# Optimization experiments

Measured on AMD Instinct MI355X. Metric: run time of the kernel, lower is better.

Reference implementation:

```python
import jax, jax.numpy as jnp
import numpy as np

RES = 512
MAX_DEPTH = 100.0
AMBIENT = 0.3
LIGHT_STREN = 0.8
SHININESS = 16.0
EPS = 1e-8


def _unit(v):
    return v / (jnp.linalg.norm(v, axis=-1, keepdims=True) + EPS)


def setup_inputs() -> dict:
    key = jax.random.key(0)
    ks = jax.random.split(key, 8)
    B, N, M, TEX = 1, 512, 128, 512
    verts = jax.random.uniform(ks[0], (B, N, 3), minval=-1.0, maxval=1.0, dtype=jnp.float32)
    faces = jax.random.randint(ks[1], (B, M, 3), 0, N, dtype=jnp.int32)
    normals = jax.random.normal(ks[2], (B, M, 3, 3), dtype=jnp.float32)
    uvs = jax.random.uniform(ks[3], (B, M, 3, 2), dtype=jnp.float32)
    textures = jax.random.uniform(ks[4], (B, TEX, TEX, 3), dtype=jnp.float32)
    f = RES / 2.0
    K = jnp.array([[f, 0.0, RES / 2.0], [0.0, f, RES / 2.0], [0.0, 0.0, 1.0]], jnp.float32)
    Ks = jnp.broadcast_to(K, (B, 3, 3))
    RT = jnp.concatenate([jnp.eye(3, dtype=jnp.float32), jnp.array([[0.0], [0.0], [2.0]], jnp.float32)], axis=1)
    RTs = jnp.broadcast_to(RT, (B, 3, 4))
    view_dir = jax.random.normal(ks[5], (B, 3), dtype=jnp.float32)
    light_dir = jax.random.normal(ks[6], (B, 3), dtype=jnp.float32)
    return {"verts": verts, "faces": faces, "normals": normals, "uvs": uvs,
            "textures": textures, "Ks": Ks, "RTs": RTs, "view_dir": view_dir, "light_dir": light_dir}


def _render(verts, faces, normals, uvs, textures, Ks, RTs, view_dir, light_dir):
    B = verts.shape[0]
    # camera space: cam = R @ v + t
    cam = jnp.einsum('bij,bnj->bni', RTs[:, :, :3], verts) + RTs[:, None, :, 3]
    # orthographic projection to pixel coords
    x = Ks[:, None, 0, 0] * cam[..., 0] + Ks[:, None, 0, 2]
    y = Ks[:, None, 1, 1] * cam[..., 1] + Ks[:, None, 1, 2]
    xy = jnp.stack([x, y], -1)            # [B,N,2]
    z = cam[..., 2]                        # [B,N]
    gather_v = jax.vmap(lambda a, f: a[f])
    tv = gather_v(xy, faces)               # [B,M,3,2] screen-space triangle corners
    tz = gather_v(z, faces)                # [B,M,3]
    # pixel centers, row-major (p = row*RES + col)
    ii = jnp.arange(RES, dtype=jnp.float32) + 0.5
    py, px = jnp.meshgrid(ii, ii, indexing='ij')
    pix = jnp.stack([px.ravel(), py.ravel()], -1)   # [P,2]

    def edge(a, b, p):
        return (b[..., 0] - a[..., 0]) * (p[..., 1] - a[..., 1]) - (b[..., 1] - a[..., 1]) * (p[..., 0] - a[..., 0])

    v0, v1, v2 = tv[:, None, :, 0], tv[:, None, :, 1], tv[:, None, :, 2]  # [B,1,M,2]
    p = pix[None, :, None]                                               # [1,P,1,2]
    w0 = edge(v1, v2, p)                   # [B,P,M]
    w1 = edge(v2, v0, p)
    w2 = edge(v0, v1, p)
    area = w0 + w1 + w2
    inside = (((w0 >= 0) & (w1 >= 0) & (w2 >= 0)) | ((w0 <= 0) & (w1 <= 0) & (w2 <= 0))) & (jnp.abs(area) > EPS)
    inv_a = 1.0 / jnp.where(jnp.abs(area) > EPS, area, 1.0)
    zpix = (w0 * tz[:, None, :, 0] + w1 * tz[:, None, :, 1] + w2 * tz[:, None, :, 2]) * inv_a
    valid = inside & (zpix > 0)
    zc = jnp.where(valid, zpix, MAX_DEPTH)   # [B,P,M] candidate depths
    depth = jnp.min(zc, axis=-1)             # z-buffer result [B,P]
    win = jnp.argmin(zc, axis=-1)             # winning triangle per pixel [B,P]
    hit = depth < MAX_DEPTH

    # recompute barycentrics for the winning triangle only (avoids [B,P,M,3])
    gpick = jax.vmap(lambda a, i: a[i])
    tvw = gpick(tv, win)                      # [B,P,3,2]
    nw = gpick(normals, win)                  # [B,P,3,3]
    uvw = gpick(uvs, win)                     # [B,P,3,2]
    pp = pix[None]                            # [1,P,2]

    def e2(a, b):
        return (b[..., 0] - a[..., 0]) * (pp[..., 1] - a[..., 1]) - (b[..., 1] - a[..., 1]) * (pp[..., 0] - a[..., 0])

    u0 = e2(tvw[:, :, 1], tvw[:, :, 2])
    u1 = e2(tvw[:, :, 2], tvw[:, :, 0])
    u2 = e2(tvw[:, :, 0], tvw[:, :, 1])
    ar = u0 + u1 + u2
    inv2 = 1.0 / jnp.where(jnp.abs(ar) > EPS, ar, 1.0)
    bary = jnp.stack([u0, u1, u2], -1) * inv2[..., None]   # [B,P,3]
    nrm = _unit(jnp.einsum('bpk,bpkc->bpc', bary, nw))     # interpolated normal
    uv = jnp.einsum('bpk,bpkc->bpc', bary, uvw)            # interpolated uv [B,P,2]

    # bilinear texture sampling
    Ht, Wt = textures.shape[1], textures.shape[2]
    uu = jnp.clip(uv[..., 0], 0.0, 1.0) * (Wt - 1)
    vv = jnp.clip(uv[..., 1], 0.0, 1.0) * (Ht - 1)
    x0 = jnp.floor(uu).astype(jnp.int32)
    y0 = jnp.floor(vv).astype(jnp.int32)
    x1 = jnp.minimum(x0 + 1, Wt - 1)
    y1 = jnp.minimum(y0 + 1, Ht - 1)
    fx = (uu - x0.astype(jnp.float32))[..., None]
    fy = (vv - y0.astype(jnp.float32))[..., None]
    tget = jax.vmap(lambda t, a, b: t[a, b])
    col = (tget(textures, y0, x0) * (1 - fx) * (1 - fy) + tget(textures, y0, x1) * fx * (1 - fy)
           + tget(textures, y1, x0) * (1 - fx) * fy + tget(textures, y1, x1) * fx * fy)  # [B,P,3]

    # Lambert diffuse + Blinn-Phong specular
    ld = _unit(light_dir)
    vd = _unit(view_dir)
    diff = jnp.clip(jnp.einsum('bpc,bc->bp', nrm, ld), 0.0)
    h = _unit(ld + vd)
    spec = LIGHT_STREN * jnp.clip(jnp.einsum('bpc,bc->bp', nrm, h), 0.0) ** SHININESS
    shade = col * (AMBIENT + LIGHT_STREN * diff)[..., None] + spec[..., None]
    rgb = jnp.where(hit[..., None], shade, 0.0)

    depths = depth.reshape(B, RES, RES)
    rgbs = rgb.reshape(B, RES, RES, 3)
    masks = hit.reshape(B, RES, RES).astype(jnp.int32)
    return depths, rgbs, masks


def reference(verts, faces, normals, uvs, textures, Ks, RTs, view_dir, light_dir):
    return _render(verts, faces, normals, uvs, textures, Ks, RTs, view_dir, light_dir)
```

## Files before the change

kernel.cpp:

```cpp
#include <hip/hip_runtime.h>
#include <math.h>

#pragma clang fp contract(off)

#define RES         512
#define TILE        16
#define TILESX      (RES / TILE)
#define MAXF        128
#define MAX_DEPTH   100.0f
#define AMBIENT     0.3f
#define LIGHT_STREN 0.8f
#define EPSF        1e-8f
#define MARG        1.0f
#define ZGUARD      1e-3f

struct __attribute__((packed, aligned(4))) PF4 { float a, b, c, d; };
struct __attribute__((packed, aligned(4))) PF2 { float a, b; };
static __device__ __forceinline__ PF4 ld4(const float* p) { PF4 v; __builtin_memcpy(&v, p, 16); return v; }
static __device__ __forceinline__ PF2 ld2(const float* p) { PF2 v; __builtin_memcpy(&v, p, 8); return v; }

__global__ __launch_bounds__(256) void mesh_render_tiled(
    const float* __restrict__ verts,
    const int*   __restrict__ faces,
    const float* __restrict__ normals,
    const float* __restrict__ uvs,
    const float* __restrict__ tex,
    const float* __restrict__ Ks,
    const float* __restrict__ RTs,
    const float* __restrict__ view_dir,
    const float* __restrict__ light_dir,
    float* __restrict__ out,
    int M, int TEXW, int TEXH)
{
    __shared__ float4 smA[MAXF];
    __shared__ float4 smB[MAXF];
    __shared__ float2 smC[MAXF];
    __shared__ int    cid[MAXF];
    __shared__ int    scnt[2][8];
    __shared__ float  slit[6];

    const int tid = threadIdx.x;
    const int tx  = blockIdx.x % TILESX;
    const int ty  = blockIdx.x / TILESX;
    const float PX0 = (float)(tx * TILE) + 0.5f;
    const float PY0 = (float)(ty * TILE) + 0.5f;

    bool flag = false;
    int  bkt  = -1;
    float X0=0,Y0=0,Z0=0, X1=0,Y1=0,Z1=0, X2=0,Y2=0,Z2=0, MZ=0;
    unsigned long long bmask = 0;

    if (tid < MAXF) {
        if (tid < M) {
            const float r00 = RTs[0], r01 = RTs[1], r02 = RTs[2],  t0 = RTs[3];
            const float r10 = RTs[4], r11 = RTs[5], r12 = RTs[6],  t1 = RTs[7];
            const float r20 = RTs[8], r21 = RTs[9], r22 = RTs[10], t2 = RTs[11];
            const float k00 = Ks[0], k02 = Ks[2], k11 = Ks[4], k12 = Ks[5];
            float X[3], Y[3], Z[3];
            #pragma unroll
            for (int k = 0; k < 3; ++k) {
                int vi = faces[tid * 3 + k];
                float vx = verts[vi * 3 + 0];
                float vy = verts[vi * 3 + 1];
                float vz = verts[vi * 3 + 2];
                float cx = ((r00 * vx + r01 * vy) + r02 * vz) + t0;
                float cy = ((r10 * vx + r11 * vy) + r12 * vz) + t1;
                float cz = ((r20 * vx + r21 * vy) + r22 * vz) + t2;
                X[k] = k00 * cx + k02;
                Y[k] = k11 * cy + k12;
                Z[k] = cz;
            }
            X0=X[0]; Y0=Y[0]; Z0=Z[0]; X1=X[1]; Y1=Y[1]; Z1=Z[1];
            X2=X[2]; Y2=Y[2]; Z2=Z[2];
            MZ = fminf(fminf(Z0, Z1), Z2);

            float e0dx = X2-X1, e0dy = Y2-Y1;
            float e1dx = X0-X2, e1dy = Y0-Y2;
            float e2dx = X1-X0, e2dy = Y1-Y0;

            float minX = fminf(fminf(X0,X1),X2), maxX = fmaxf(fmaxf(X0,X1),X2);
            float minY = fminf(fminf(Y0,Y1),Y2), maxY = fmaxf(fmaxf(Y0,Y1),Y2);
            bool bb = (minX <= PX0 + 15.0f + MARG) && (maxX >= PX0 - MARG) &&
                      (minY <= PY0 + 15.0f + MARG) && (maxY >= PY0 - MARG);

            float wA0 = e0dx*(PY0-Y1) - e0dy*(PX0-X1);
            float wA1 = e1dx*(PY0-Y2) - e1dy*(PX0-X2);
            float wA2 = e2dx*(PY0-Y0) - e2dy*(PX0-X0);
            float area = (wA0 + wA1) + wA2;
            float amin = fminf(area, 0.0f) - MARG, amax = fmaxf(area, 0.0f) + MARG;

            float s0x = -e0dy*15.0f, s0y = e0dx*15.0f;
            float s1x = -e1dy*15.0f, s1y = e1dx*15.0f;
            float s2x = -e2dy*15.0f, s2y = e2dx*15.0f;
            float t0min = wA0 + fminf(s0x,0.f) + fminf(s0y,0.f);
            float t0max = wA0 + fmaxf(s0x,0.f) + fmaxf(s0y,0.f);
            float t1min = wA1 + fminf(s1x,0.f) + fminf(s1y,0.f);
            float t1max = wA1 + fmaxf(s1x,0.f) + fmaxf(s1y,0.f);
            float t2min = wA2 + fminf(s2x,0.f) + fminf(s2y,0.f);
            float t2max = wA2 + fmaxf(s2x,0.f) + fmaxf(s2y,0.f);
            bool ok0 = (t0max >= amin) && (t0min <= amax);
            bool ok1 = (t1max >= amin) && (t1min <= amax);
            bool ok2 = (t2max >= amin) && (t2min <= amax);
            flag = bb && ok0 && ok1 && ok2;
            if (flag) {
                int bq = (int)((MZ - 1.0f) * 4.0f);
                bkt = bq < 0 ? 0 : (bq > 7 ? 7 : bq);
            }
        }
        #pragma unroll
        for (int k = 0; k < 8; ++k) {
            unsigned long long mk = __ballot(flag && (bkt == k));
            if (bkt == k) bmask = mk;
            if ((tid & 63) == 0) scnt[tid >> 6][k] = __popcll(mk);
        }
    }
    if (tid == 128) {
        float lx = light_dir[0], ly = light_dir[1], lz = light_dir[2];
        float ll = sqrtf((lx*lx + ly*ly) + lz*lz) + 1e-8f;
        lx /= ll; ly /= ll; lz /= ll;
        float vx = view_dir[0], vy = view_dir[1], vz = view_dir[2];
        float vl = sqrtf((vx*vx + vy*vy) + vz*vz) + 1e-8f;
        vx /= vl; vy /= vl; vz /= vl;
        float hx = lx + vx, hy = ly + vy, hz = lz + vz;
        float hl = sqrtf((hx*hx + hy*hy) + hz*hz) + 1e-8f;
        slit[0] = lx; slit[1] = ly; slit[2] = lz;
        slit[3] = hx / hl; slit[4] = hy / hl; slit[5] = hz / hl;
    }
    __syncthreads();

    if (flag) {
        int wv = tid >> 6;
        int base = 0;
        for (int k = 0; k < bkt; ++k) base += scnt[0][k] + scnt[1][k];
        if (wv == 1) base += scnt[0][bkt];
        int pos = base + __popcll(bmask & ((1ull << (tid & 63)) - 1ull));
        smA[pos] = make_float4(X0, Y0, X1, Y1);
        smB[pos] = make_float4(X2, Y2, Z0, Z1);
        smC[pos] = make_float2(MZ - ZGUARD, Z2);
        cid[pos] = tid;
    }
    __syncthreads();

    int bend[8];
    {
        int acc = 0;
        #pragma unroll
        for (int k = 0; k < 8; ++k) { acc += scnt[0][k] + scnt[1][k]; bend[k] = acc; }
    }

    const int lx_ = tid & (TILE-1), ly_ = tid / TILE;
    const float px = PX0 + (float)lx_;
    const float py = PY0 + (float)ly_;
    const int p = (ty*TILE + ly_) * RES + (tx*TILE + lx_);

    float best = MAX_DEPTH;
    float w0s = 0.0f, w1s = 0.0f, w2s = 0.0f, invs = 1.0f;
    int winpos = -1;

    int i = 0;
    #pragma unroll 1
    for (int k = 0; k < 8; ++k) {
        const int e = bend[k];
        if (i >= e) continue;
        float lbk = (1.0f + 0.25f * (float)k) - ZGUARD;
        if (__all(lbk >= best)) break;
        for (; i < e; ++i) {
            const float2 c = smC[i];
            if (__all(c.x >= best)) continue;
            const float4 A = smA[i];
            const float4 B = smB[i];
            float w0 = (B.x - A.z) * (py - A.w) - (B.y - A.w) * (px - A.z);
            float w1 = (A.x - B.x) * (py - B.y) - (A.y - B.y) * (px - B.x);
            float w2 = (A.z - A.x) * (py - A.y) - (A.w - A.y) * (px - A.x);
            float area = (w0 + w1) + w2;
            float mn = fminf(fminf(w0, w1), w2);
            float mx = fmaxf(fmaxf(w0, w1), w2);
            bool nz = fabsf(area) > EPSF;
            bool inside = ((mn >= 0.0f) || (mx <= 0.0f)) && nz;
            float inva = __builtin_amdgcn_rcpf(nz ? area : 1.0f);
            float zpix = ((w0 * B.z + w1 * B.w) + w2 * c.y) * inva;
            float zc = (inside && (zpix > 0.0f)) ? zpix : MAX_DEPTH;
            if (zc < best) {
                best = zc; winpos = i;
                w0s = w0; w1s = w1; w2s = w2; invs = inva;
            }
        }
    }

    float r = 0.0f, g = 0.0f, b = 0.0f, mk = 0.0f, depth = MAX_DEPTH;
    if (winpos >= 0) {
        mk = 1.0f;
        depth = best;
        const int f = cid[winpos];
        float b0 = w0s * invs, b1 = w1s * invs, b2 = w2s * invs;

        const float* nw = normals + f * 9;
        PF4 n0 = ld4(nw); PF4 n1 = ld4(nw + 4); float n8 = nw[8];
        float nx  = (b0 * n0.a + b1 * n0.d) + b2 * n1.c;
        float ny  = (b0 * n0.b + b1 * n1.a) + b2 * n1.d;
        float nzv = (b0 * n0.c + b1 * n1.b) + b2 * n8;
        float nl  = __builtin_amdgcn_sqrtf((nx*nx + ny*ny) + nzv*nzv) + 1e-8f;
        float rn  = __builtin_amdgcn_rcpf(nl);
        nx *= rn; ny *= rn; nzv *= rn;

        const float* uvp = uvs + f * 6;
        PF4 u0 = ld4(uvp); PF2 u1 = ld2(uvp + 4);
        float uvx = (b0 * u0.a + b1 * u0.c) + b2 * u1.a;
        float uvy = (b0 * u0.b + b1 * u0.d) + b2 * u1.b;
        float uu = fminf(fmaxf(uvx, 0.0f), 1.0f) * (float)(TEXW - 1);
        float vv = fminf(fmaxf(uvy, 0.0f), 1.0f) * (float)(TEXH - 1);
        int x0 = (int)floorf(uu), y0 = (int)floorf(vv);
        int y1 = min(y0 + 1, TEXH - 1);
        float fx = uu - (float)x0, fy = vv - (float)y0;

        int xb = min(x0, TEXW - 2);
        bool xe = (x0 == TEXW - 1);
        const float* r0 = tex + (y0 * TEXW + xb) * 3;
        const float* r1 = tex + (y1 * TEXW + xb) * 3;
        PF4 a0 = ld4(r0); PF2 a1 = ld2(r0 + 4);
        PF4 c0 = ld4(r1); PF2 c1 = ld2(r1 + 4);
        float t00r = xe ? a0.d : a0.a, t00g = xe ? a1.a : a0.b, t00b = xe ? a1.b : a0.c;
        float t01r = a0.d,             t01g = a1.a,             t01b = a1.b;
        float t10r = xe ? c0.d : c0.a, t10g = xe ? c1.a : c0.b, t10b = xe ? c1.b : c0.c;
        float t11r = c0.d,             t11g = c1.a,             t11b = c1.b;

        float gx = 1.0f - fx, gy = 1.0f - fy;
        float cr = (((t00r*gx)*gy + (t01r*fx)*gy) + (t10r*gx)*fy) + (t11r*fx)*fy;
        float cg = (((t00g*gx)*gy + (t01g*fx)*gy) + (t10g*gx)*fy) + (t11g*fx)*fy;
        float cb = (((t00b*gx)*gy + (t01b*fx)*gy) + (t10b*gx)*fy) + (t11b*fx)*fy;

        float ldx = slit[0], ldy = slit[1], ldz = slit[2];
        float hx  = slit[3], hy  = slit[4], hz  = slit[5];
        float diff = fmaxf((nx*ldx + ny*ldy) + nzv*ldz, 0.0f);
        float sd   = fmaxf((nx*hx  + ny*hy)  + nzv*hz,  0.0f);
        float s2 = sd*sd, s4 = s2*s2, s8 = s4*s4, s16 = s8*s8;
        float spec  = LIGHT_STREN * s16;
        float scale = AMBIENT + LIGHT_STREN * diff;
        r = cr * scale + spec;
        g = cg * scale + spec;
        b = cb * scale + spec;
    }

    out[p] = depth;
    struct F3 { float x, y, z; };
    ((F3*)(out + RES * RES))[p] = F3{r, g, b};
    out[RES * RES * 4 + p] = mk;
}

extern "C" void kernel_launch(void* const* d_in, const int* in_sizes, int n_in,
                              void* d_out, int out_size, void* d_ws, size_t ws_size,
                              hipStream_t stream) {
    const float* verts     = (const float*)d_in[0];
    const int*   faces     = (const int*)  d_in[1];
    const float* normals   = (const float*)d_in[2];
    const float* uvs       = (const float*)d_in[3];
    const float* tex       = (const float*)d_in[4];
    const float* Ks        = (const float*)d_in[5];
    const float* RTs       = (const float*)d_in[6];
    const float* view_dir  = (const float*)d_in[7];
    const float* light_dir = (const float*)d_in[8];

    int M = in_sizes[1] / 3;
    if (M > MAXF) M = MAXF;
    const int texels = in_sizes[4] / 3;
    const int TEXW = (int)(sqrt((double)texels) + 0.5);
    const int TEXH = TEXW;

    const int blocks = TILESX * TILESX;
    mesh_render_tiled<<<blocks, 256, 0, stream>>>(
        verts, faces, normals, uvs, tex, Ks, RTs, view_dir, light_dir,
        (float*)d_out, M, TEXW, TEXH);
}
```

Before: 16.21 us.

## Split vertex transform into prepass kernel and rasterize 8x8 tiles with single-wave blocks

```diff
diff --git a/kernel.cpp b/kernel.cpp
--- a/kernel.cpp
+++ b/kernel.cpp
@@ -4,7 +4,7 @@
 #pragma clang fp contract(off)
 
 #define RES         512
-#define TILE        16
+#define TILE        8
 #define TILESX      (RES / TILE)
 #define MAXF        128
 #define MAX_DEPTH   100.0f
@@ -13,20 +13,51 @@
 #define EPSF        1e-8f
 #define MARG        1.0f
 #define ZGUARD      1e-3f
+#define EXT         7.0f
 
 struct __attribute__((packed, aligned(4))) PF4 { float a, b, c, d; };
 struct __attribute__((packed, aligned(4))) PF2 { float a, b; };
 static __device__ __forceinline__ PF4 ld4(const float* p) { PF4 v; __builtin_memcpy(&v, p, 16); return v; }
 static __device__ __forceinline__ PF2 ld2(const float* p) { PF2 v; __builtin_memcpy(&v, p, 8); return v; }
 
-__global__ __launch_bounds__(256) void mesh_render_tiled(
-    const float* __restrict__ verts,
-    const int*   __restrict__ faces,
+__global__ __launch_bounds__(128) void xform_faces(
+    const float* __restrict__ verts, const int* __restrict__ faces,
+    const float* __restrict__ Ks, const float* __restrict__ RTs,
+    float4* __restrict__ ws, int M)
+{
+    const int f = threadIdx.x;
+    if (f >= M) return;
+    const float r00 = RTs[0], r01 = RTs[1], r02 = RTs[2],  t0 = RTs[3];
+    const float r10 = RTs[4], r11 = RTs[5], r12 = RTs[6],  t1 = RTs[7];
+    const float r20 = RTs[8], r21 = RTs[9], r22 = RTs[10], t2 = RTs[11];
+    const float k00 = Ks[0], k02 = Ks[2], k11 = Ks[4], k12 = Ks[5];
+    float X[3], Y[3], Z[3];
+    #pragma unroll
+    for (int k = 0; k < 3; ++k) {
+        int vi = faces[f * 3 + k];
+        float vx = verts[vi * 3 + 0];
+        float vy = verts[vi * 3 + 1];
+        float vz = verts[vi * 3 + 2];
+        float cx = ((r00 * vx + r01 * vy) + r02 * vz) + t0;
+        float cy = ((r10 * vx + r11 * vy) + r12 * vz) + t1;
+        float cz = ((r20 * vx + r21 * vy) + r22 * vz) + t2;
+        X[k] = k00 * cx + k02;
+        Y[k] = k11 * cy + k12;
+        Z[k] = cz;
+    }
+    float MZ = fminf(fminf(Z[0], Z[1]), Z[2]);
+    int bq = (int)((MZ - 1.0f) * 4.0f);
+    int bkt = bq < 0 ? 0 : (bq > 7 ? 7 : bq);
+    ws[f * 3 + 0] = make_float4(X[0], Y[0], X[1], Y[1]);
+    ws[f * 3 + 1] = make_float4(X[2], Y[2], Z[0], Z[1]);
+    ws[f * 3 + 2] = make_float4(MZ - ZGUARD, Z[2], (float)bkt, 0.0f);
+}
+
+__global__ __launch_bounds__(64) void raster_tiles(
+    const float4* __restrict__ ws,
     const float* __restrict__ normals,
     const float* __restrict__ uvs,
     const float* __restrict__ tex,
-    const float* __restrict__ Ks,
-    const float* __restrict__ RTs,
     const float* __restrict__ view_dir,
     const float* __restrict__ light_dir,
     float* __restrict__ out,
@@ -36,117 +67,76 @@
     __shared__ float4 smB[MAXF];
     __shared__ float2 smC[MAXF];
     __shared__ int    cid[MAXF];
-    __shared__ int    scnt[2][8];
-    __shared__ float  slit[6];
 
     const int tid = threadIdx.x;
-    const int tx  = blockIdx.x % TILESX;
+    const int tx  = blockIdx.x & (TILESX - 1);
     const int ty  = blockIdx.x / TILESX;
     const float PX0 = (float)(tx * TILE) + 0.5f;
     const float PY0 = (float)(ty * TILE) + 0.5f;
 
-    bool flag = false;
-    int  bkt  = -1;
-    float X0=0,Y0=0,Z0=0, X1=0,Y1=0,Z1=0, X2=0,Y2=0,Z2=0, MZ=0;
-    unsigned long long bmask = 0;
-
-    if (tid < MAXF) {
-        if (tid < M) {
-            const float r00 = RTs[0], r01 = RTs[1], r02 = RTs[2],  t0 = RTs[3];
-            const float r10 = RTs[4], r11 = RTs[5], r12 = RTs[6],  t1 = RTs[7];
-            const float r20 = RTs[8], r21 = RTs[9], r22 = RTs[10], t2 = RTs[11];
-            const float k00 = Ks[0], k02 = Ks[2], k11 = Ks[4], k12 = Ks[5];
-            float X[3], Y[3], Z[3];
-            #pragma unroll
-            for (int k = 0; k < 3; ++k) {
-                int vi = faces[tid * 3 + k];
-                float vx = verts[vi * 3 + 0];
-                float vy = verts[vi * 3 + 1];
-                float vz = verts[vi * 3 + 2];
-                float cx = ((r00 * vx + r01 * vy) + r02 * vz) + t0;
-                float cy = ((r10 * vx + r11 * vy) + r12 * vz) + t1;
-                float cz = ((r20 * vx + r21 * vy) + r22 * vz) + t2;
-                X[k] = k00 * cx + k02;
-                Y[k] = k11 * cy + k12;
-                Z[k] = cz;
-            }
-            X0=X[0]; Y0=Y[0]; Z0=Z[0]; X1=X[1]; Y1=Y[1]; Z1=Z[1];
-            X2=X[2]; Y2=Y[2]; Z2=Z[2];
-            MZ = fminf(fminf(Z0, Z1), Z2);
-
-            float e0dx = X2-X1, e0dy = Y2-Y1;
-            float e1dx = X0-X2, e1dy = Y0-Y2;
-            float e2dx = X1-X0, e2dy = Y1-Y0;
-
-            float minX = fminf(fminf(X0,X1),X2), maxX = fmaxf(fmaxf(X0,X1),X2);
-            float minY = fminf(fminf(Y0,Y1),Y2), maxY = fmaxf(fmaxf(Y0,Y1),Y2);
-            bool bb = (minX <= PX0 + 15.0f + MARG) && (maxX >= PX0 - MARG) &&
-                      (minY <= PY0 + 15.0f + MARG) && (maxY >= PY0 - MARG);
-
-            float wA0 = e0dx*(PY0-Y1) - e0dy*(PX0-X1);
-            float wA1 = e1dx*(PY0-Y2) - e1dy*(PX0-X2);
-            float wA2 = e2dx*(PY0-Y0) - e2dy*(PX0-X0);
-            float area = (wA0 + wA1) + wA2;
-            float amin = fminf(area, 0.0f) - MARG, amax = fmaxf(area, 0.0f) + MARG;
-
-            float s0x = -e0dy*15.0f, s0y = e0dx*15.0f;
-            float s1x = -e1dy*15.0f, s1y = e1dx*15.0f;
-            float s2x = -e2dy*15.0f, s2y = e2dx*15.0f;
-            float t0min = wA0 + fminf(s0x,0.f) + fminf(s0y,0.f);
-            float t0max = wA0 + fmaxf(s0x,0.f) + fmaxf(s0y,0.f);
-            float t1min = wA1 + fminf(s1x,0.f) + fminf(s1y,0.f);
-            float t1max = wA1 + fmaxf(s1x,0.f) + fmaxf(s1y,0.f);
-            float t2min = wA2 + fminf(s2x,0.f) + fminf(s2y,0.f);
-            float t2max = wA2 + fmaxf(s2x,0.f) + fmaxf(s2y,0.f);
-            bool ok0 = (t0max >= amin) && (t0min <= amax);
-            bool ok1 = (t1max >= amin) && (t1min <= amax);
-            bool ok2 = (t2max >= amin) && (t2min <= amax);
-            flag = bb && ok0 && ok1 && ok2;
-            if (flag) {
-                int bq = (int)((MZ - 1.0f) * 4.0f);
-                bkt = bq < 0 ? 0 : (bq > 7 ? 7 : bq);
-            }
-        }
-        #pragma unroll
-        for (int k = 0; k < 8; ++k) {
-            unsigned long long mk = __ballot(flag && (bkt == k));
-            if (bkt == k) bmask = mk;
-            if ((tid & 63) == 0) scnt[tid >> 6][k] = __popcll(mk);
-        }
-    }
-    if (tid == 128) {
-        float lx = light_dir[0], ly = light_dir[1], lz = light_dir[2];
-        float ll = sqrtf((lx*lx + ly*ly) + lz*lz) + 1e-8f;
-        lx /= ll; ly /= ll; lz /= ll;
-        float vx = view_dir[0], vy = view_dir[1], vz = view_dir[2];
-        float vl = sqrtf((vx*vx + vy*vy) + vz*vz) + 1e-8f;
-        vx /= vl; vy /= vl; vz /= vl;
-        float hx = lx + vx, hy = ly + vy, hz = lz + vz;
-        float hl = sqrtf((hx*hx + hy*hy) + hz*hz) + 1e-8f;
-        slit[0] = lx; slit[1] = ly; slit[2] = lz;
-        slit[3] = hx / hl; slit[4] = hy / hl; slit[5] = hz / hl;
-    }
+    const int f0 = tid, f1 = tid + 64;
+    float4 A0 = ws[f0 * 3 + 0], B0 = ws[f0 * 3 + 1], C0 = ws[f0 * 3 + 2];
+    float4 A1, B1, C1;
+    bool have1 = (f1 < M);
+    if (have1) { A1 = ws[f1 * 3 + 0]; B1 = ws[f1 * 3 + 1]; C1 = ws[f1 * 3 + 2]; }
+
+    auto sat = [&](const float4& A, const float4& B) -> bool {
+        float e0dx = B.x - A.z, e0dy = B.y - A.w;
+        float e1dx = A.x - B.x, e1dy = A.y - B.y;
+        float e2dx = A.z - A.x, e2dy = A.w - A.y;
+        float minX = fminf(fminf(A.x, A.z), B.x), maxX = fmaxf(fmaxf(A.x, A.z), B.x);
+        float minY = fminf(fminf(A.y, A.w), B.y), maxY = fmaxf(fmaxf(A.y, A.w), B.y);
+        bool bb = (minX <= PX0 + EXT + MARG) && (maxX >= PX0 - MARG) &&
+                  (minY <= PY0 + EXT + MARG) && (maxY >= PY0 - MARG);
+        float wA0 = e0dx*(PY0 - A.w) - e0dy*(PX0 - A.z);
+        float wA1 = e1dx*(PY0 - B.y) - e1dy*(PX0 - B.x);
+        float wA2 = e2dx*(PY0 - A.y) - e2dy*(PX0 - A.x);
+        float area = (wA0 + wA1) + wA2;
+        float amin = fminf(area, 0.0f) - MARG, amax = fmaxf(area, 0.0f) + MARG;
+        float s0x = -e0dy*EXT, s0y = e0dx*EXT;
+        float s1x = -e1dy*EXT, s1y = e1dx*EXT;
+        float s2x = -e2dy*EXT, s2y = e2dx*EXT;
+        float t0mn = wA0 + fminf(s0x,0.f) + fminf(s0y,0.f);
+        float t0mx = wA0 + fmaxf(s0x,0.f) + fmaxf(s0y,0.f);
+        float t1mn = wA1 + fminf(s1x,0.f) + fminf(s1y,0.f);
+        float t1mx = wA1 + fmaxf(s1x,0.f) + fmaxf(s1y,0.f);
+        float t2mn = wA2 + fminf(s2x,0.f) + fminf(s2y,0.f);
+        float t2mx = wA2 + fmaxf(s2x,0.f) + fmaxf(s2y,0.f);
+        bool ok0 = (t0mx >= amin) && (t0mn <= amax);
+        bool ok1 = (t1mx >= amin) && (t1mn <= amax);
+        bool ok2 = (t2mx >= amin) && (t2mn <= amax);
+        return bb && ok0 && ok1 && ok2;
+    };
+    bool flag0 = (f0 < M) && sat(A0, B0);
+    bool flag1 = have1 && sat(A1, B1);
+    int bkt0 = flag0 ? (int)C0.z : -1;
+    int bkt1 = flag1 ? (int)C1.z : -1;
+
+    const unsigned long long lt = (1ull << tid) - 1ull;
+    int posA = -1, posB = -1, bend[8];
+    int acc = 0;
+    #pragma unroll
+    for (int k = 0; k < 8; ++k) {
+        unsigned long long mA = __ballot(bkt0 == k);
+        unsigned long long mB = __ballot(bkt1 == k);
+        if (bkt0 == k) posA = acc + __popcll(mA & lt);
+        if (bkt1 == k) posB = acc + __popcll(mA) + __popcll(mB & lt);
+        acc += __popcll(mA) + __popcll(mB);
+        bend[k] = acc;
+    }
+    if (posA >= 0) { smA[posA]=A0; smB[posA]=B0; smC[posA]=make_float2(C0.x,C0.y); cid[posA]=f0; }
+    if (posB >= 0) { smA[posB]=A1; smB[posB]=B1; smC[posB]=make_float2(C1.x,C1.y); cid[posB]=f1; }
     __syncthreads();
 
-    if (flag) {
-        int wv = tid >> 6;
-        int base = 0;
-        for (int k = 0; k < bkt; ++k) base += scnt[0][k] + scnt[1][k];
-        if (wv == 1) base += scnt[0][bkt];
-        int pos = base + __popcll(bmask & ((1ull << (tid & 63)) - 1ull));
-        smA[pos] = make_float4(X0, Y0, X1, Y1);
-        smB[pos] = make_float4(X2, Y2, Z0, Z1);
-        smC[pos] = make_float2(MZ - ZGUARD, Z2);
-        cid[pos] = tid;
-    }
-    __syncthreads();
-
-    int bend[8];
-    {
-        int acc = 0;
-        #pragma unroll
-        for (int k = 0; k < 8; ++k) { acc += scnt[0][k] + scnt[1][k]; bend[k] = acc; }
-    }
+    float ldx = light_dir[0], ldy = light_dir[1], ldz = light_dir[2];
+    float ll = sqrtf((ldx*ldx + ldy*ldy) + ldz*ldz) + 1e-8f;
+    ldx /= ll; ldy /= ll; ldz /= ll;
+    float vx = view_dir[0], vy = view_dir[1], vz = view_dir[2];
+    float vl = sqrtf((vx*vx + vy*vy) + vz*vz) + 1e-8f;
+    vx /= vl; vy /= vl; vz /= vl;
+    float hx = ldx + vx, hy = ldy + vy, hz = ldz + vz;
+    float hl = sqrtf((hx*hx + hy*hy) + hz*hz) + 1e-8f;
+    hx /= hl; hy /= hl; hz /= hl;
 
     const int lx_ = tid & (TILE-1), ly_ = tid / TILE;
     const float px = PX0 + (float)lx_;
@@ -229,8 +219,6 @@
         float cg = (((t00g*gx)*gy + (t01g*fx)*gy) + (t10g*gx)*fy) + (t11g*fx)*fy;
         float cb = (((t00b*gx)*gy + (t01b*fx)*gy) + (t10b*gx)*fy) + (t11b*fx)*fy;
 
-        float ldx = slit[0], ldy = slit[1], ldz = slit[2];
-        float hx  = slit[3], hy  = slit[4], hz  = slit[5];
         float diff = fmaxf((nx*ldx + ny*ldy) + nzv*ldz, 0.0f);
         float sd   = fmaxf((nx*hx  + ny*hy)  + nzv*hz,  0.0f);
         float s2 = sd*sd, s4 = s2*s2, s8 = s4*s4, s16 = s8*s8;
@@ -266,8 +254,10 @@
     const int TEXW = (int)(sqrt((double)texels) + 0.5);
     const int TEXH = TEXW;
 
+    float4* ws = (float4*)d_ws;
+    xform_faces<<<1, 128, 0, stream>>>(verts, faces, Ks, RTs, ws, M);
     const int blocks = TILESX * TILESX;
-    mesh_render_tiled<<<blocks, 256, 0, stream>>>(
-        verts, faces, normals, uvs, tex, Ks, RTs, view_dir, light_dir,
+    raster_tiles<<<blocks, 64, 0, stream>>>(
+        ws, normals, uvs, tex, view_dir, light_dir,
         (float*)d_out, M, TEXW, TEXH);
 }
```

Result: slower. 20.84 us (+28.6%).

## Halve block size, shade two pixels per thread, stage verts/faces in LDS

Applied to the files above, without the earlier changes.

```diff
diff --git a/kernel.cpp b/kernel.cpp
--- a/kernel.cpp
+++ b/kernel.cpp
@@ -7,6 +7,7 @@
 #define TILE        16
 #define TILESX      (RES / TILE)
 #define MAXF        128
+#define MAXV        512
 #define MAX_DEPTH   100.0f
 #define AMBIENT     0.3f
 #define LIGHT_STREN 0.8f
@@ -19,7 +20,7 @@
 static __device__ __forceinline__ PF4 ld4(const float* p) { PF4 v; __builtin_memcpy(&v, p, 16); return v; }
 static __device__ __forceinline__ PF2 ld2(const float* p) { PF2 v; __builtin_memcpy(&v, p, 8); return v; }
 
-__global__ __launch_bounds__(256) void mesh_render_tiled(
+__global__ __launch_bounds__(128) void mesh_render_tiled(
     const float* __restrict__ verts,
     const int*   __restrict__ faces,
     const float* __restrict__ normals,
@@ -30,14 +31,15 @@
     const float* __restrict__ view_dir,
     const float* __restrict__ light_dir,
     float* __restrict__ out,
-    int M, int TEXW, int TEXH)
+    int M, int NV, int TEXW, int TEXH)
 {
+    __shared__ float sverts[MAXV * 3];
+    __shared__ int   sfaces[MAXF * 3];
     __shared__ float4 smA[MAXF];
     __shared__ float4 smB[MAXF];
     __shared__ float2 smC[MAXF];
     __shared__ int    cid[MAXF];
     __shared__ int    scnt[2][8];
-    __shared__ float  slit[6];
 
     const int tid = threadIdx.x;
     const int tx  = blockIdx.x % TILESX;
@@ -45,86 +47,90 @@
     const float PX0 = (float)(tx * TILE) + 0.5f;
     const float PY0 = (float)(ty * TILE) + 0.5f;
 
+    {
+        const int nvf = NV * 3;
+        const int nv4 = nvf >> 2;
+        const float4* v4 = (const float4*)verts;
+        for (int idx = tid; idx < nv4; idx += 128)
+            ((float4*)sverts)[idx] = v4[idx];
+        for (int idx = (nv4 << 2) + tid; idx < nvf; idx += 128)
+            sverts[idx] = verts[idx];
+        const int nff = M * 3;
+        const int nf4 = nff >> 2;
+        const int4* f4 = (const int4*)faces;
+        for (int idx = tid; idx < nf4; idx += 128)
+            ((int4*)sfaces)[idx] = f4[idx];
+        for (int idx = (nf4 << 2) + tid; idx < nff; idx += 128)
+            sfaces[idx] = faces[idx];
+    }
+    __syncthreads();
+
     bool flag = false;
     int  bkt  = -1;
     float X0=0,Y0=0,Z0=0, X1=0,Y1=0,Z1=0, X2=0,Y2=0,Z2=0, MZ=0;
     unsigned long long bmask = 0;
 
-    if (tid < MAXF) {
-        if (tid < M) {
-            const float r00 = RTs[0], r01 = RTs[1], r02 = RTs[2],  t0 = RTs[3];
-            const float r10 = RTs[4], r11 = RTs[5], r12 = RTs[6],  t1 = RTs[7];
-            const float r20 = RTs[8], r21 = RTs[9], r22 = RTs[10], t2 = RTs[11];
-            const float k00 = Ks[0], k02 = Ks[2], k11 = Ks[4], k12 = Ks[5];
-            float X[3], Y[3], Z[3];
-            #pragma unroll
-            for (int k = 0; k < 3; ++k) {
-                int vi = faces[tid * 3 + k];
-                float vx = verts[vi * 3 + 0];
-                float vy = verts[vi * 3 + 1];
-                float vz = verts[vi * 3 + 2];
-                float cx = ((r00 * vx + r01 * vy) + r02 * vz) + t0;
-                float cy = ((r10 * vx + r11 * vy) + r12 * vz) + t1;
-                float cz = ((r20 * vx + r21 * vy) + r22 * vz) + t2;
-                X[k] = k00 * cx + k02;
-                Y[k] = k11 * cy + k12;
-                Z[k] = cz;
-            }
-            X0=X[0]; Y0=Y[0]; Z0=Z[0]; X1=X[1]; Y1=Y[1]; Z1=Z[1];
-            X2=X[2]; Y2=Y[2]; Z2=Z[2];
-            MZ = fminf(fminf(Z0, Z1), Z2);
-
-            float e0dx = X2-X1, e0dy = Y2-Y1;
-            float e1dx = X0-X2, e1dy = Y0-Y2;
-            float e2dx = X1-X0, e2dy = Y1-Y0;
-
-            float minX = fminf(fminf(X0,X1),X2), maxX = fmaxf(fmaxf(X0,X1),X2);
-            float minY = fminf(fminf(Y0,Y1),Y2), maxY = fmaxf(fmaxf(Y0,Y1),Y2);
-            bool bb = (minX <= PX0 + 15.0f + MARG) && (maxX >= PX0 - MARG) &&
-                      (minY <= PY0 + 15.0f + MARG) && (maxY >= PY0 - MARG);
-
-            float wA0 = e0dx*(PY0-Y1) - e0dy*(PX0-X1);
-            float wA1 = e1dx*(PY0-Y2) - e1dy*(PX0-X2);
-            float wA2 = e2dx*(PY0-Y0) - e2dy*(PX0-X0);
-            float area = (wA0 + wA1) + wA2;
-            float amin = fminf(area, 0.0f) - MARG, amax = fmaxf(area, 0.0f) + MARG;
-
-            float s0x = -e0dy*15.0f, s0y = e0dx*15.0f;
-            float s1x = -e1dy*15.0f, s1y = e1dx*15.0f;
-            float s2x = -e2dy*15.0f, s2y = e2dx*15.0f;
-            float t0min = wA0 + fminf(s0x,0.f) + fminf(s0y,0.f);
-            float t0max = wA0 + fmaxf(s0x,0.f) + fmaxf(s0y,0.f);
-            float t1min = wA1 + fminf(s1x,0.f) + fminf(s1y,0.f);
-            float t1max = wA1 + fmaxf(s1x,0.f) + fmaxf(s1y,0.f);
-            float t2min = wA2 + fminf(s2x,0.f) + fminf(s2y,0.f);
-            float t2max = wA2 + fmaxf(s2x,0.f) + fmaxf(s2y,0.f);
-            bool ok0 = (t0max >= amin) && (t0min <= amax);
-            bool ok1 = (t1max >= amin) && (t1min <= amax);
-            bool ok2 = (t2max >= amin) && (t2min <= amax);
-            flag = bb && ok0 && ok1 && ok2;
-            if (flag) {
-                int bq = (int)((MZ - 1.0f) * 4.0f);
-                bkt = bq < 0 ? 0 : (bq > 7 ? 7 : bq);
-            }
+    if (tid < M) {
+        const float r00 = RTs[0], r01 = RTs[1], r02 = RTs[2],  t0 = RTs[3];
+        const float r10 = RTs[4], r11 = RTs[5], r12 = RTs[6],  t1 = RTs[7];
+        const float r20 = RTs[8], r21 = RTs[9], r22 = RTs[10], t2 = RTs[11];
+        const float k00 = Ks[0], k02 = Ks[2], k11 = Ks[4], k12 = Ks[5];
+        float X[3], Y[3], Z[3];
+        #pragma unroll
+        for (int k = 0; k < 3; ++k) {
+            int vi = sfaces[tid * 3 + k];
+            float vx = sverts[vi * 3 + 0];
+            float vy = sverts[vi * 3 + 1];
+            float vz = sverts[vi * 3 + 2];
+            float cx = ((r00 * vx + r01 * vy) + r02 * vz) + t0;
+            float cy = ((r10 * vx + r11 * vy) + r12 * vz) + t1;
+            float cz = ((r20 * vx + r21 * vy) + r22 * vz) + t2;
+            X[k] = k00 * cx + k02;
+            Y[k] = k11 * cy + k12;
+            Z[k] = cz;
         }
-        #pragma unroll
-        for (int k = 0; k < 8; ++k) {
-            unsigned long long mk = __ballot(flag && (bkt == k));
-            if (bkt == k) bmask = mk;
-            if ((tid & 63) == 0) scnt[tid >> 6][k] = __popcll(mk);
+        X0=X[0]; Y0=Y[0]; Z0=Z[0]; X1=X[1]; Y1=Y[1]; Z1=Z[1];
+        X2=X[2]; Y2=Y[2]; Z2=Z[2];
+        MZ = fminf(fminf(Z0, Z1), Z2);
+
+        float e0dx = X2-X1, e0dy = Y2-Y1;
+        float e1dx = X0-X2, e1dy = Y0-Y2;
+        float e2dx = X1-X0, e2dy = Y1-Y0;
+
+        float minX = fminf(fminf(X0,X1),X2), maxX = fmaxf(fmaxf(X0,X1),X2);
+        float minY = fminf(fminf(Y0,Y1),Y2), maxY = fmaxf(fmaxf(Y0,Y1),Y2);
+        bool bb = (minX <= PX0 + 15.0f + MARG) && (maxX >= PX0 - MARG) &&
+                  (minY <= PY0 + 15.0f + MARG) && (maxY >= PY0 - MARG);
+
+        float wA0 = e0dx*(PY0-Y1) - e0dy*(PX0-X1);
+        float wA1 = e1dx*(PY0-Y2) - e1dy*(PX0-X2);
+        float wA2 = e2dx*(PY0-Y0) - e2dy*(PX0-X0);
+        float area = (wA0 + wA1) + wA2;
+        float amin = fminf(area, 0.0f) - MARG, amax = fmaxf(area, 0.0f) + MARG;
+
+        float s0x = -e0dy*15.0f, s0y = e0dx*15.0f;
+        float s1x = -e1dy*15.0f, s1y = e1dx*15.0f;
+        float s2x = -e2dy*15.0f, s2y = e2dx*15.0f;
+        float t0mn = wA0 + fminf(s0x,0.f) + fminf(s0y,0.f);
+        float t0mx = wA0 + fmaxf(s0x,0.f) + fmaxf(s0y,0.f);
+        float t1mn = wA1 + fminf(s1x,0.f) + fminf(s1y,0.f);
+        float t1mx = wA1 + fmaxf(s1x,0.f) + fmaxf(s1y,0.f);
+        float t2mn = wA2 + fminf(s2x,0.f) + fminf(s2y,0.f);
+        float t2mx = wA2 + fmaxf(s2x,0.f) + fmaxf(s2y,0.f);
+        bool ok0 = (t0mx >= amin) && (t0mn <= amax);
+        bool ok1 = (t1mx >= amin) && (t1mn <= amax);
+        bool ok2 = (t2mx >= amin) && (t2mn <= amax);
+        flag = bb && ok0 && ok1 && ok2;
+        if (flag) {
+            int bq = (int)((MZ - 1.0f) * 4.0f);
+            bkt = bq < 0 ? 0 : (bq > 7 ? 7 : bq);
         }
     }
-    if (tid == 128) {
-        float lx = light_dir[0], ly = light_dir[1], lz = light_dir[2];
-        float ll = sqrtf((lx*lx + ly*ly) + lz*lz) + 1e-8f;
-        lx /= ll; ly /= ll; lz /= ll;
-        float vx = view_dir[0], vy = view_dir[1], vz = view_dir[2];
-        float vl = sqrtf((vx*vx + vy*vy) + vz*vz) + 1e-8f;
-        vx /= vl; vy /= vl; vz /= vl;
-        float hx = lx + vx, hy = ly + vy, hz = lz + vz;
-        float hl = sqrtf((hx*hx + hy*hy) + hz*hz) + 1e-8f;
-        slit[0] = lx; slit[1] = ly; slit[2] = lz;
-        slit[3] = hx / hl; slit[4] = hy / hl; slit[5] = hz / hl;
+    #pragma unroll
+    for (int k = 0; k < 8; ++k) {
+        unsigned long long mk = __ballot(flag && (bkt == k));
+        if (bkt == k) bmask = mk;
+        if ((tid & 63) == 0) scnt[tid >> 6][k] = __popcll(mk);
     }
     __syncthreads();
 
@@ -148,14 +154,27 @@
         for (int k = 0; k < 8; ++k) { acc += scnt[0][k] + scnt[1][k]; bend[k] = acc; }
     }
 
-    const int lx_ = tid & (TILE-1), ly_ = tid / TILE;
-    const float px = PX0 + (float)lx_;
-    const float py = PY0 + (float)ly_;
-    const int p = (ty*TILE + ly_) * RES + (tx*TILE + lx_);
-
-    float best = MAX_DEPTH;
-    float w0s = 0.0f, w1s = 0.0f, w2s = 0.0f, invs = 1.0f;
-    int winpos = -1;
+    float ldx = light_dir[0], ldy = light_dir[1], ldz = light_dir[2];
+    float ll = sqrtf((ldx*ldx + ldy*ldy) + ldz*ldz) + 1e-8f;
+    ldx /= ll; ldy /= ll; ldz /= ll;
+    float vdx = view_dir[0], vdy = view_dir[1], vdz = view_dir[2];
+    float vl = sqrtf((vdx*vdx + vdy*vdy) + vdz*vdz) + 1e-8f;
+    vdx /= vl; vdy /= vl; vdz /= vl;
+    float hx = ldx + vdx, hy = ldy + vdy, hz = ldz + vdz;
+    float hl = sqrtf((hx*hx + hy*hy) + hz*hz) + 1e-8f;
+    hx /= hl; hy /= hl; hz /= hl;
+
+    const int lx_ = tid & (TILE-1), ly_ = tid >> 4;
+    const float px  = PX0 + (float)lx_;
+    const float pyA = PY0 + (float)ly_;
+    const float pyB = pyA + 8.0f;
+    const int pA = (ty*TILE + ly_) * RES + (tx*TILE + lx_);
+    const int pB = pA + 8 * RES;
+
+    float bestA = MAX_DEPTH, bestB = MAX_DEPTH;
+    float wA0s=0, wA1s=0, wA2s=0, invAs=1.0f;
+    float wB0s=0, wB1s=0, wB2s=0, invBs=1.0f;
+    int winA = -1, winB = -1;
 
     int i = 0;
     #pragma unroll 1
@@ -163,88 +182,114 @@
         const int e = bend[k];
         if (i >= e) continue;
         float lbk = (1.0f + 0.25f * (float)k) - ZGUARD;
-        if (__all(lbk >= best)) break;
+        if (__all(lbk >= fmaxf(bestA, bestB))) break;
         for (; i < e; ++i) {
             const float2 c = smC[i];
-            if (__all(c.x >= best)) continue;
+            if (__all(c.x >= fmaxf(bestA, bestB))) continue;
             const float4 A = smA[i];
             const float4 B = smB[i];
-            float w0 = (B.x - A.z) * (py - A.w) - (B.y - A.w) * (px - A.z);
-            float w1 = (A.x - B.x) * (py - B.y) - (A.y - B.y) * (px - B.x);
-            float w2 = (A.z - A.x) * (py - A.y) - (A.w - A.y) * (px - A.x);
-            float area = (w0 + w1) + w2;
-            float mn = fminf(fminf(w0, w1), w2);
-            float mx = fmaxf(fmaxf(w0, w1), w2);
-            bool nz = fabsf(area) > EPSF;
-            bool inside = ((mn >= 0.0f) || (mx <= 0.0f)) && nz;
-            float inva = __builtin_amdgcn_rcpf(nz ? area : 1.0f);
-            float zpix = ((w0 * B.z + w1 * B.w) + w2 * c.y) * inva;
-            float zc = (inside && (zpix > 0.0f)) ? zpix : MAX_DEPTH;
-            if (zc < best) {
-                best = zc; winpos = i;
-                w0s = w0; w1s = w1; w2s = w2; invs = inva;
+            {
+                float w0 = (B.x - A.z) * (pyA - A.w) - (B.y - A.w) * (px - A.z);
+                float w1 = (A.x - B.x) * (pyA - B.y) - (A.y - B.y) * (px - B.x);
+                float w2 = (A.z - A.x) * (pyA - A.y) - (A.w - A.y) * (px - A.x);
+                float area = (w0 + w1) + w2;
+                float mn = fminf(fminf(w0, w1), w2);
+                float mx = fmaxf(fmaxf(w0, w1), w2);
+                bool nz = fabsf(area) > EPSF;
+                bool inside = ((mn >= 0.0f) || (mx <= 0.0f)) && nz;
+                float inva = __builtin_amdgcn_rcpf(nz ? area : 1.0f);
+                float zpix = ((w0 * B.z + w1 * B.w) + w2 * c.y) * inva;
+                float zc = (inside && (zpix > 0.0f)) ? zpix : MAX_DEPTH;
+                if (zc < bestA) {
+                    bestA = zc; winA = i;
+                    wA0s = w0; wA1s = w1; wA2s = w2; invAs = inva;
+                }
+            }
+            {
+                float w0 = (B.x - A.z) * (pyB - A.w) - (B.y - A.w) * (px - A.z);
+                float w1 = (A.x - B.x) * (pyB - B.y) - (A.y - B.y) * (px - B.x);
+                float w2 = (A.z - A.x) * (pyB - A.y) - (A.w - A.y) * (px - A.x);
+                float area = (w0 + w1) + w2;
+                float mn = fminf(fminf(w0, w1), w2);
+                float mx = fmaxf(fmaxf(w0, w1), w2);
+                bool nz = fabsf(area) > EPSF;
+                bool inside = ((mn >= 0.0f) || (mx <= 0.0f)) && nz;
+                float inva = __builtin_amdgcn_rcpf(nz ? area : 1.0f);
+                float zpix = ((w0 * B.z + w1 * B.w) + w2 * c.y) * inva;
+                float zc = (inside && (zpix > 0.0f)) ? zpix : MAX_DEPTH;
+                if (zc < bestB) {
+                    bestB = zc; winB = i;
+                    wB0s = w0; wB1s = w1; wB2s = w2; invBs = inva;
+                }
             }
         }
     }
 
-    float r = 0.0f, g = 0.0f, b = 0.0f, mk = 0.0f, depth = MAX_DEPTH;
-    if (winpos >= 0) {
-        mk = 1.0f;
-        depth = best;
-        const int f = cid[winpos];
-        float b0 = w0s * invs, b1 = w1s * invs, b2 = w2s * invs;
-
-        const float* nw = normals + f * 9;
-        PF4 n0 = ld4(nw); PF4 n1 = ld4(nw + 4); float n8 = nw[8];
-        float nx  = (b0 * n0.a + b1 * n0.d) + b2 * n1.c;
-        float ny  = (b0 * n0.b + b1 * n1.a) + b2 * n1.d;
-        float nzv = (b0 * n0.c + b1 * n1.b) + b2 * n8;
-        float nl  = __builtin_amdgcn_sqrtf((nx*nx + ny*ny) + nzv*nzv) + 1e-8f;
-        float rn  = __builtin_amdgcn_rcpf(nl);
-        nx *= rn; ny *= rn; nzv *= rn;
-
-        const float* uvp = uvs + f * 6;
-        PF4 u0 = ld4(uvp); PF2 u1 = ld2(uvp + 4);
-        float uvx = (b0 * u0.a + b1 * u0.c) + b2 * u1.a;
-        float uvy = (b0 * u0.b + b1 * u0.d) + b2 * u1.b;
-        float uu = fminf(fmaxf(uvx, 0.0f), 1.0f) * (float)(TEXW - 1);
-        float vv = fminf(fmaxf(uvy, 0.0f), 1.0f) * (float)(TEXH - 1);
-        int x0 = (int)floorf(uu), y0 = (int)floorf(vv);
-        int y1 = min(y0 + 1, TEXH - 1);
-        float fx = uu - (float)x0, fy = vv - (float)y0;
-
-        int xb = min(x0, TEXW - 2);
-        bool xe = (x0 == TEXW - 1);
-        const float* r0 = tex + (y0 * TEXW + xb) * 3;
-        const float* r1 = tex + (y1 * TEXW + xb) * 3;
-        PF4 a0 = ld4(r0); PF2 a1 = ld2(r0 + 4);
-        PF4 c0 = ld4(r1); PF2 c1 = ld2(r1 + 4);
-        float t00r = xe ? a0.d : a0.a, t00g = xe ? a1.a : a0.b, t00b = xe ? a1.b : a0.c;
-        float t01r = a0.d,             t01g = a1.a,             t01b = a1.b;
-        float t10r = xe ? c0.d : c0.a, t10g = xe ? c1.a : c0.b, t10b = xe ? c1.b : c0.c;
-        float t11r = c0.d,             t11g = c1.a,             t11b = c1.b;
-
-        float gx = 1.0f - fx, gy = 1.0f - fy;
-        float cr = (((t00r*gx)*gy + (t01r*fx)*gy) + (t10r*gx)*fy) + (t11r*fx)*fy;
-        float cg = (((t00g*gx)*gy + (t01g*fx)*gy) + (t10g*gx)*fy) + (t11g*fx)*fy;
-        float cb = (((t00b*gx)*gy + (t01b*fx)*gy) + (t10b*gx)*fy) + (t11b*fx)*fy;
-
-        float ldx = slit[0], ldy = slit[1], ldz = slit[2];
-        float hx  = slit[3], hy  = slit[4], hz  = slit[5];
-        float diff = fmaxf((nx*ldx + ny*ldy) + nzv*ldz, 0.0f);
-        float sd   = fmaxf((nx*hx  + ny*hy)  + nzv*hz,  0.0f);
-        float s2 = sd*sd, s4 = s2*s2, s8 = s4*s4, s16 = s8*s8;
-        float spec  = LIGHT_STREN * s16;
-        float scale = AMBIENT + LIGHT_STREN * diff;
-        r = cr * scale + spec;
-        g = cg * scale + spec;
-        b = cb * scale + spec;
-    }
-
-    out[p] = depth;
-    struct F3 { float x, y, z; };
-    ((F3*)(out + RES * RES))[p] = F3{r, g, b};
-    out[RES * RES * 4 + p] = mk;
+    #pragma unroll
+    for (int q = 0; q < 2; ++q) {
+        const int   winpos = q ? winB : winA;
+        const float best   = q ? bestB : bestA;
+        const float w0s = q ? wB0s : wA0s, w1s = q ? wB1s : wA1s;
+        const float w2s = q ? wB2s : wA2s, invs = q ? invBs : invAs;
+        const int   p   = q ? pB : pA;
+
+        float r = 0.0f, g = 0.0f, b = 0.0f, mk = 0.0f, depth = MAX_DEPTH;
+        if (winpos >= 0) {
+            mk = 1.0f;
+            depth = best;
+            const int f = cid[winpos];
+            float b0 = w0s * invs, b1 = w1s * invs, b2 = w2s * invs;
+
+            const float* nw = normals + f * 9;
+            PF4 n0 = ld4(nw); PF4 n1 = ld4(nw + 4); float n8 = nw[8];
+            float nx  = (b0 * n0.a + b1 * n0.d) + b2 * n1.c;
+            float ny  = (b0 * n0.b + b1 * n1.a) + b2 * n1.d;
+            float nzv = (b0 * n0.c + b1 * n1.b) + b2 * n8;
+            float nl  = __builtin_amdgcn_sqrtf((nx*nx + ny*ny) + nzv*nzv) + 1e-8f;
+            float rn  = __builtin_amdgcn_rcpf(nl);
+            nx *= rn; ny *= rn; nzv *= rn;
+
+            const float* uvp = uvs + f * 6;
+            PF4 u0 = ld4(uvp); PF2 u1 = ld2(uvp + 4);
+            float uvx = (b0 * u0.a + b1 * u0.c) + b2 * u1.a;
+            float uvy = (b0 * u0.b + b1 * u0.d) + b2 * u1.b;
+            float uu = fminf(fmaxf(uvx, 0.0f), 1.0f) * (float)(TEXW - 1);
+            float vv = fminf(fmaxf(uvy, 0.0f), 1.0f) * (float)(TEXH - 1);
+            int x0 = (int)floorf(uu), y0 = (int)floorf(vv);
+            int y1 = min(y0 + 1, TEXH - 1);
+            float fx = uu - (float)x0, fy = vv - (float)y0;
+
+            int xb = min(x0, TEXW - 2);
+            bool xe = (x0 == TEXW - 1);
+            const float* r0 = tex + (y0 * TEXW + xb) * 3;
+            const float* r1 = tex + (y1 * TEXW + xb) * 3;
+            PF4 a0 = ld4(r0); PF2 a1 = ld2(r0 + 4);
+            PF4 c0 = ld4(r1); PF2 c1 = ld2(r1 + 4);
+            float t00r = xe ? a0.d : a0.a, t00g = xe ? a1.a : a0.b, t00b = xe ? a1.b : a0.c;
+            float t01r = a0.d,             t01g = a1.a,             t01b = a1.b;
+            float t10r = xe ? c0.d : c0.a, t10g = xe ? c1.a : c0.b, t10b = xe ? c1.b : c0.c;
+            float t11r = c0.d,             t11g = c1.a,             t11b = c1.b;
+
+            float gx = 1.0f - fx, gy = 1.0f - fy;
+            float cr = (((t00r*gx)*gy + (t01r*fx)*gy) + (t10r*gx)*fy) + (t11r*fx)*fy;
+            float cg = (((t00g*gx)*gy + (t01g*fx)*gy) + (t10g*gx)*fy) + (t11g*fx)*fy;
+            float cb = (((t00b*gx)*gy + (t01b*fx)*gy) + (t10b*gx)*fy) + (t11b*fx)*fy;
+
+            float diff = fmaxf((nx*ldx + ny*ldy) + nzv*ldz, 0.0f);
+            float sd   = fmaxf((nx*hx  + ny*hy)  + nzv*hz,  0.0f);
+            float s2 = sd*sd, s4 = s2*s2, s8 = s4*s4, s16 = s8*s8;
+            float spec  = LIGHT_STREN * s16;
+            float scale = AMBIENT + LIGHT_STREN * diff;
+            r = cr * scale + spec;
+            g = cg * scale + spec;
+            b = cb * scale + spec;
+        }
+
+        out[p] = depth;
+        struct F3 { float x, y, z; };
+        ((F3*)(out + RES * RES))[p] = F3{r, g, b};
+        out[RES * RES * 4 + p] = mk;
+    }
 }
 
 extern "C" void kernel_launch(void* const* d_in, const int* in_sizes, int n_in,
@@ -262,12 +307,14 @@
 
     int M = in_sizes[1] / 3;
     if (M > MAXF) M = MAXF;
+    int NV = in_sizes[0] / 3;
+    if (NV > MAXV) NV = MAXV;
     const int texels = in_sizes[4] / 3;
     const int TEXW = (int)(sqrt((double)texels) + 0.5);
     const int TEXH = TEXW;
 
     const int blocks = TILESX * TILESX;
-    mesh_render_tiled<<<blocks, 256, 0, stream>>>(
+    mesh_render_tiled<<<blocks, 128, 0, stream>>>(
         verts, faces, normals, uvs, tex, Ks, RTs, view_dir, light_dir,
-        (float*)d_out, M, TEXW, TEXH);
+        (float*)d_out, M, NV, TEXW, TEXH);
 }
```

Measured after the change: 20.19 us. 24.6% more time.
